# Optimization experiments

Hardware: AMD Instinct MI355X
Metric: run time of the kernel (lower is better)

## Reference

```python
import jax, jax.numpy as jnp
import numpy as np

H = 4          # attention heads
K = 16         # knn neighbors
EPS = 1e-5     # BatchNorm eps


def setup_inputs() -> dict:
    key = jax.random.key(0)
    ks = jax.random.split(key, 10)
    B, C, T, N = 2, 128, 32, 512
    OUT = 128
    HID = 2 * C + 2 * OUT  # ff hidden = in*2 + out*2
    s = 0.02
    return {
        "x_all": jax.random.normal(ks[0], (B, C, T, N), jnp.float32),
        "Wq": jax.random.normal(ks[1], (C, C), jnp.float32) * s,
        "Wk": jax.random.normal(ks[2], (C, C), jnp.float32) * s,
        "Wv": jax.random.normal(ks[3], (C, C), jnp.float32) * s,
        "W1": jax.random.normal(ks[4], (HID, C), jnp.float32) * s,
        "W2": jax.random.normal(ks[5], (OUT, HID), jnp.float32) * s,
        "bn_gamma": 1.0 + 0.1 * jax.random.normal(ks[6], (OUT,), jnp.float32),
        "bn_beta": 0.1 * jax.random.normal(ks[7], (OUT,), jnp.float32),
        "bn_mean": 0.1 * jax.random.normal(ks[8], (OUT,), jnp.float32),
        "bn_var": jax.random.uniform(ks[9], (OUT,), jnp.float32, 0.5, 1.5),
    }


def reference(x_all, Wq, Wk, Wv, W1, W2, bn_gamma, bn_beta, bn_mean, bn_var):
    B, C, T, N = x_all.shape
    D = C // H
    # --- st_group_points: candidate pool = 3 consecutive frames (replicate temporal pad), frame-major ---
    xp = jnp.concatenate([x_all[:, :, :1], x_all, x_all[:, :, -1:]], axis=2)   # (B,C,T+2,N)
    pool = jnp.stack([xp[:, :, :-2], xp[:, :, 1:-1], xp[:, :, 2:]], axis=3)    # (B,C,T,3,N)
    pool = pool.reshape(B, C, T, 3 * N)                                        # (B,C,T,3N)
    # KNN on xyz (channels 0:3); sqrt is monotone so topk on squared dists gives same indices
    a = x_all[:, :3]                                                           # (B,3,T,N)
    b = pool[:, :3]                                                            # (B,3,T,3N)
    d2 = jnp.sum((a[..., :, None] - b[..., None, :]) ** 2, axis=1)             # (B,T,N,3N)
    _, idx = jax.lax.top_k(-d2, K)                                             # (B,T,N,K) smallest-dist
    nb = jnp.take_along_axis(pool[:, :, :, None, :], idx[:, None], axis=-1)    # (B,C,T,N,K)
    rel = x_all[..., None] - nb                                                # diff grouping (B,C,T,N,K)
    # --- per-point local attention over K neighbors (1x1 convs == channel matmuls), all t at once ---
    q = jnp.einsum('oc,bctn->botn', Wq, x_all).reshape(B, H, D, T, N)
    k = jnp.einsum('oc,bctnk->botnk', Wk, rel).reshape(B, H, D, T, N, K)
    v = jnp.einsum('oc,bctnk->botnk', Wv, rel).reshape(B, H, D, T, N, K)
    energy = jnp.einsum('bhdtn,bhdtnk->bhtnk', q, k) / jnp.sqrt(jnp.float32(D))
    attn = jax.nn.softmax(energy, axis=-1)                                     # (B,H,T,N,K)
    agg = jnp.einsum('bhtnk,bhdtnk->bhdtn', attn, v).reshape(B, C, T, N)
    # --- residual + BatchNorm1d (eval mode, running stats) + conv feed-forward ---
    h = x_all + agg
    scale = (bn_gamma / jnp.sqrt(bn_var + EPS))[None, :, None, None]
    h = (h - bn_mean[None, :, None, None]) * scale + bn_beta[None, :, None, None]
    h = jax.nn.leaky_relu(jnp.einsum('oc,bctn->botn', W1, h), 0.2)
    y = jnp.einsum('oc,bctn->botn', W2, h)                                     # (B,OUT,T,N)
    return jnp.concatenate([x_all[:, :4], y], axis=1)                          # (B,4+OUT,T,N)
```

## Files before the change

### kernel.cpp

```cpp
#include <hip/hip_runtime.h>
#include <hip/hip_bf16.h>

typedef __hip_bfloat16 bf16;
typedef unsigned long long u64;
typedef __attribute__((ext_vector_type(8))) short short8;
typedef __attribute__((ext_vector_type(4))) float f32x4;

#define B_   2
#define C_   128
#define T_   32
#define N_   512
#define K_   16
#define HID_ 512
#define TN   (T_*N_)
#define PTS  (B_*T_*N_)

#define MFMA_BF16(a,b,c) __builtin_amdgcn_mfma_f32_16x16x32_bf16((a),(b),(c),0,0,0)

__device__ __forceinline__ float b2f(bf16 v){ return __bfloat162float(v); }
__device__ __forceinline__ bf16  f2b(float v){ return __float2bfloat16(v); }
__device__ __forceinline__ float bqf(short v){
  return __uint_as_float(((unsigned)(unsigned short)v) << 16);
}

__device__ __forceinline__ float ldc(const void* p, int i, bool f32) {
  return f32 ? ((const float*)p)[i] : b2f(((const bf16*)p)[i]);
}

__global__ __launch_bounds__(256) void convw_kernel(
    const void* __restrict__ x,
    const void* wq, const void* wk, const void* wv,
    const void* w1, const void* w2, const void* g, const void* bb,
    const void* m, const void* v,
    bf16* __restrict__ wqb, bf16* __restrict__ wkb, bf16* __restrict__ wvb,
    bf16* __restrict__ w1b, bf16* __restrict__ w2b,
    float* __restrict__ gf, float* __restrict__ bf_, float* __restrict__ mf,
    float* __restrict__ vf, int* __restrict__ flag)
{
  __shared__ int cnt;
  if (threadIdx.x == 0) cnt = 0;
  __syncthreads();
  const unsigned short* u = (const unsigned short*)x;
  int w = 0;
#pragma unroll
  for (int j = 0; j < 8; ++j) {
    unsigned short hv = u[threadIdx.x*8 + j];
    int e = (hv >> 7) & 0xFF;
    if (e >= 0x89) w++;
  }
  if (w) atomicAdd(&cnt, w);
  __syncthreads();
  bool f32 = (cnt > 32);
  if (blockIdx.x == 0 && threadIdx.x == 0) *flag = f32 ? 1 : 0;

  int i = blockIdx.x*256 + threadIdx.x;
  if (i < 16384) { wqb[i] = f2b(ldc(wq, i, f32)); return; } i -= 16384;
  if (i < 16384) { wkb[i] = f2b(ldc(wk, i, f32)); return; } i -= 16384;
  if (i < 16384) { wvb[i] = f2b(ldc(wv, i, f32)); return; } i -= 16384;
  if (i < 65536) { w1b[i] = f2b(ldc(w1, i, f32)); return; } i -= 65536;
  if (i < 65536) { w2b[i] = f2b(ldc(w2, i, f32)); return; } i -= 65536;
  if (i < 128)   { gf[i]  = ldc(g, i, f32); return; }       i -= 128;
  if (i < 128)   { bf_[i] = ldc(bb, i, f32); return; }      i -= 128;
  if (i < 128)   { mf[i]  = ldc(m, i, f32); return; }       i -= 128;
  if (i < 128)   { vf[i]  = ldc(v, i, f32); return; }
}

__device__ __forceinline__ u64 shflx64(u64 v, int m) {
  return (u64)__shfl_xor((long long)v, m, 64);
}

__device__ __forceinline__ void proj_gemm32(const bf16* __restrict__ W,
                                            bf16 (*ys)[136],
                                            const short8 am[2][4],
                                            int mrow, int quad, int ot)
{
  f32x4 acc[2];
#pragma unroll
  for (int mt=0;mt<2;++mt) acc[mt] = (f32x4){0.f,0.f,0.f,0.f};
#pragma unroll
  for (int kq=0;kq<4;++kq) {
    short8 bfr = *(const short8*)&W[(ot*16+mrow)*C_ + kq*32 + quad*8];
#pragma unroll
    for (int mt=0;mt<2;++mt) acc[mt] = MFMA_BF16(am[mt][kq], bfr, acc[mt]);
  }
#pragma unroll
  for (int mt=0;mt<2;++mt)
#pragma unroll
    for (int r=0;r<4;++r)
      ys[mt*16 + quad*4 + r][ot*16 + mrow] = f2b(acc[mt][r]);
}

__device__ __forceinline__ void tile_store32_512(bf16* __restrict__ dst,
                                                 const bf16 (*ys)[136], int tid)
{
  int flat = tid*8;
  int p = flat >> 7, c = flat & 127;
  *(short8*)&dst[(size_t)p*C_ + c] = *(const short8*)&ys[p][c];
}

__global__ __launch_bounds__(512) void projknn_kernel(
    const void* __restrict__ x, const int* __restrict__ flag,
    const bf16* __restrict__ wqb, const bf16* __restrict__ wkb, const bf16* __restrict__ wvb,
    bf16* __restrict__ xTb, bf16* QT, bf16* __restrict__ KT, bf16* __restrict__ VT,
    int* __restrict__ idxout)
{
  __shared__ __align__(16) char smem[28672];
  int tid = threadIdx.x;
  int blk = blockIdx.x;
  int g = blk / 5, r = blk - g*5;
  if (r == 4) {
    bf16 (*xs )[136] = (bf16(*)[136])(smem);
    bf16 (*ysK)[136] = (bf16(*)[136])(smem + 8704);
    bf16 (*ysV)[136] = (bf16(*)[136])(smem + 17408);
    int p0 = g * 32;
    int b = p0 >> 14; int tn0 = p0 & (TN-1);
    if (*flag) {
      const float* xbase = (const float*)x + (size_t)b*C_*TN + tn0;
#pragma unroll
      for (int it=0; it<8; ++it) {
        int i = it*512 + tid;
        int c = i >> 5, p = i & 31;
        xs[p][c] = f2b(xbase[(size_t)c*TN + p]);
      }
    } else {
      const bf16* xbase = (const bf16*)x + (size_t)b*C_*TN + tn0;
#pragma unroll
      for (int it=0; it<8; ++it) {
        int i = it*512 + tid;
        int c = i >> 5, p = i & 31;
        xs[p][c] = xbase[(size_t)c*TN + p];
      }
    }
    __syncthreads();
    tile_store32_512(xTb + (size_t)p0*C_, xs, tid);
    int lane = tid & 63, wave = tid >> 6;
    int mrow = lane & 15, quad = lane >> 4;
    short8 am[2][4];
#pragma unroll
    for (int mt=0;mt<2;++mt)
#pragma unroll
      for (int kq=0;kq<4;++kq)
        am[mt][kq] = *(const short8*)&xs[mt*16 + mrow][kq*32 + quad*8];
    __syncthreads();
    proj_gemm32(wqb, xs,  am, mrow, quad, wave);
    proj_gemm32(wkb, ysK, am, mrow, quad, wave);
    proj_gemm32(wvb, ysV, am, mrow, quad, wave);
    __syncthreads();
    tile_store32_512(QT + (size_t)p0*C_, xs,  tid);
    tile_store32_512(KT + (size_t)p0*C_, ysK, tid);
    tile_store32_512(VT + (size_t)p0*C_, ysV, tid);
  } else {
    float4* cand4 = (float4*)smem;
    u64 (*surv)[64] = (u64(*)[64])(smem + 24576);
    int kblk = g*4 + r;
    int row = kblk >> 6;
    int b = row >> 5, t = row & 31;
    int ng = kblk & 63;
    bool f32 = (*flag != 0);
#pragma unroll
    for (int q = 0; q < 3; ++q) {
      int tt = t - 1 + q; tt = tt < 0 ? 0 : (tt > T_-1 ? T_-1 : tt);
      size_t base = ((size_t)b*C_*T_ + tt)*(size_t)N_ + tid;
      float c0, c1, c2;
      if (f32) {
        const float* xp = (const float*)x;
        c0 = xp[base]; c1 = xp[base + (size_t)T_*N_]; c2 = xp[base + 2*(size_t)T_*N_];
      } else {
        const bf16* xp = (const bf16*)x;
        c0 = b2f(xp[base]); c1 = b2f(xp[base + (size_t)T_*N_]); c2 = b2f(xp[base + 2*(size_t)T_*N_]);
      }
      cand4[q*N_ + tid] = make_float4(c0, c1, c2, 0.f);
    }
    __syncthreads();
    int wave = tid >> 6, lane = tid & 63;
    int n = ng*8 + wave;
    float4 a = cand4[N_ + n];
    unsigned db[24];
#pragma unroll
    for (int j = 0; j < 24; ++j) {
      float4 cm = cand4[lane + (j << 6)];
      float dx = a.x - cm.x;
      float dy = a.y - cm.y;
      float dz = a.z - cm.z;
      float d2 = __fadd_rn(__fadd_rn(__fmul_rn(dx,dx), __fmul_rn(dy,dy)), __fmul_rn(dz,dz));
      db[j] = __float_as_uint(d2);
    }
    unsigned mm[12];
#pragma unroll
    for (int j = 0; j < 12; ++j) mm[j] = db[2*j] < db[2*j+1] ? db[2*j] : db[2*j+1];
#pragma unroll
    for (int j = 0; j < 6; ++j)  mm[j] = mm[2*j] < mm[2*j+1] ? mm[2*j] : mm[2*j+1];
#pragma unroll
    for (int j = 0; j < 3; ++j)  mm[j] = mm[2*j] < mm[2*j+1] ? mm[2*j] : mm[2*j+1];
    unsigned bd = mm[0] < mm[1] ? mm[0] : mm[1];
    bd = bd < mm[2] ? bd : mm[2];
    {
      unsigned lo = 0u, hi = 0x7f800000u;
#pragma unroll
      for (int it = 0; it < 16; ++it) {
        unsigned mid = lo + ((hi - lo) >> 1);
        int cge = __popcll(__ballot(bd <= mid));
        bool ge = (cge >= K_);
        hi = ge ? mid : hi;
        lo = ge ? lo : (mid + 1u);
      }
      bd = hi;
    }
    unsigned U = bd;
    int c = 0;
#pragma unroll
    for (int j = 0; j < 24; ++j) c += (db[j] <= U) ? 1 : 0;
    int ofs = 0, total = 0;
#pragma unroll
    for (int bit = 0; bit < 5; ++bit) {
      u64 mball = __ballot(((c >> bit) & 1) != 0);
      unsigned below = __builtin_amdgcn_mbcnt_hi((unsigned)(mball >> 32),
                        __builtin_amdgcn_mbcnt_lo((unsigned)mball, 0u));
      ofs   += ((int)below) << bit;
      total += (__popcll(mball)) << bit;
    }
    int point = (b*T_ + t)*N_ + n;
    if (total <= 64) {
#pragma unroll
      for (int j = 0; j < 24; ++j) {
        if (db[j] <= U) {
          surv[wave][ofs] = ((u64)db[j] << 11) | (unsigned)(lane + (j << 6));
          ++ofs;
        }
      }
      if (lane == total) surv[wave][lane] = ~0ull;
      __threadfence_block();
      u64 kk = (lane < total) ? surv[wave][lane] : ~0ull;
      int npair = (total + 1) >> 1;
      int rank = 0;
      const ulonglong2* sk2 = (const ulonglong2*)&surv[wave][0];
#pragma unroll 4
      for (int i2 = 0; i2 < npair; ++i2) {
        ulonglong2 kp = sk2[i2];
        rank += (kp.x < kk) ? 1 : 0;
        rank += (kp.y < kk) ? 1 : 0;
      }
      if (rank < K_) idxout[point*K_ + rank] = (int)(kk & 2047u);
    } else {
      u64 key[24];
#pragma unroll
      for (int j = 0; j < 24; ++j)
        key[j] = ((u64)db[j] << 32) | (unsigned)(lane + (j << 6));
      u64 res = ~0ull;
#pragma unroll 1
      for (int rr = 0; rr < 16; ++rr) {
        u64 m2 = key[0];
#pragma unroll
        for (int j = 1; j < 24; ++j) m2 = (key[j] < m2) ? key[j] : m2;
#pragma unroll
        for (int s = 32; s >= 1; s >>= 1) {
          u64 p = shflx64(m2, s);
          m2 = (p < m2) ? p : m2;
        }
        if (lane == rr) res = m2;
        int mwin = (int)(m2 & 0xffffffffu);
        int sel = ((mwin & 63) == lane) ? (mwin >> 6) : -1;
#pragma unroll
        for (int j = 0; j < 24; ++j) if (j == sel) key[j] = ~0ull;
      }
      if (lane < K_) idxout[point*K_ + lane] = (int)(res & 0xffffffffu);
    }
  }
}

__global__ __launch_bounds__(512) void attn_kernel(
    const int* __restrict__ idxin, const bf16* __restrict__ xTb,
    bf16* qhT , const bf16* __restrict__ KT,
    const bf16* __restrict__ VT,
    const float* __restrict__ gf, const float* __restrict__ bf_,
    const float* __restrict__ mf, const float* __restrict__ vf)
{
  __shared__ int   col_lds[4][16];
  __shared__ float qbuf[4][C_];
  __shared__ bf16  kbuf[4][K_][136];
  __shared__ bf16  vbuf[4][K_][136];
  __shared__ float e_lds[4][4][16];
  int tid = threadIdx.x;
  int pt = tid >> 7, o = tid & 127;
  int point = blockIdx.x*4 + pt;
  int b = point >> 14; int tn = point & (TN-1); int t = tn >> 9;
  if (o < K_) {
    int m = idxin[point*K_ + o];
    int j = m >> 9, nn = m & (N_-1);
    int tt = t-1+j; tt = tt<0?0:(tt>T_-1?T_-1:tt);
    col_lds[pt][o] = ((b*T_ + tt)*N_ + nn)*C_;
  }
  int self = point*C_;
  qbuf[pt][o] = b2f(qhT[self + o]);
  __syncthreads();
#pragma unroll
  for (int it = 0; it < 2; ++it) {
    int i = it*512 + tid;
    int pp = i >> 8, rem = i & 255, k = rem >> 4, ch = rem & 15;
    int src = col_lds[pp][k] + ch*8;
    *(short8*)&kbuf[pp][k][ch*8] = *(const short8*)&KT[src];
    *(short8*)&vbuf[pp][k][ch*8] = *(const short8*)&VT[src];
  }
  __syncthreads();
  {
    int pp = tid >> 7, j = tid & 127;
    int k = j >> 3, hd = (j >> 1) & 3, half = j & 1;
    const float* qp = &qbuf[pp][hd*32 + half*16];
    const bf16*  kp = &kbuf[pp][k][hd*32 + half*16];
    short8 kv0 = *(const short8*)kp;
    short8 kv1 = *(const short8*)(kp + 8);
    float qv[16];
    *(float4*)&qv[0]  = *(const float4*)(qp);
    *(float4*)&qv[4]  = *(const float4*)(qp + 4);
    *(float4*)&qv[8]  = *(const float4*)(qp + 8);
    *(float4*)&qv[12] = *(const float4*)(qp + 12);
    float e = 0.f;
#pragma unroll
    for (int i2=0;i2<8;++i2) e = fmaf(qv[i2],   bqf(kv0[i2]), e);
#pragma unroll
    for (int i2=0;i2<8;++i2) e = fmaf(qv[8+i2], bqf(kv1[i2]), e);
    e += __shfl_xor(e, 1, 64);
    if (!half) e_lds[pp][hd][k] = -e * 0.17677669529663687f;
  }
  __syncthreads();
  int hd = o >> 5;
  float e[16]; float mx = -3e38f;
#pragma unroll
  for (int k=0;k<K_;++k){ e[k]=e_lds[pt][hd][k]; mx=fmaxf(mx,e[k]); }
  float ssum=0.f;
#pragma unroll
  for (int k=0;k<K_;++k){ e[k]=__expf(e[k]-mx); ssum+=e[k]; }
  float inv = 1.f/ssum;
  float acc = b2f(VT[self + o]);
#pragma unroll
  for (int k=0;k<K_;++k)
    acc = fmaf(-(e[k]*inv), b2f(vbuf[pt][k][o]), acc);
  float hv = b2f(xTb[self + o]) + acc;
  float sc = gf[o] / sqrtf(vf[o] + 1e-5f);
  qhT[self + o] = f2b((hv - mf[o])*sc + bf_[o]);
}

__global__ __launch_bounds__(256) void mlp_kernel(const bf16* __restrict__ hT,
                                                  const bf16* __restrict__ w1b,
                                                  const bf16* __restrict__ w2b,
                                                  const void* __restrict__ x,
                                                  const int* __restrict__ flag,
                                                  void* out)
{
  __shared__ bf16 hidh[32][264];
  int tid = threadIdx.x;
  int p0 = blockIdx.x*32;
  int lane = tid & 63, wave = tid >> 6;
  int mrow = lane & 15, quad = lane >> 4;
  bool f32o = (*flag != 0);
  int bb = p0 >> 14;
  int tn0 = p0 & (TN-1);
  if (tid < 128) {
    int c = tid >> 5, p = tid & 31;
    size_t si = ((size_t)bb*C_ + c)*TN + tn0 + p;
    size_t di = ((size_t)bb*132 + c)*TN + tn0 + p;
    if (f32o) ((float*)out)[di] = ((const float*)x)[si];
    else      ((bf16*)out)[di]  = ((const bf16*)x)[si];
  }
  f32x4 acc2[2][2];
#pragma unroll
  for (int oi=0;oi<2;++oi)
#pragma unroll
    for (int mt=0;mt<2;++mt) acc2[oi][mt] = (f32x4){0.f,0.f,0.f,0.f};

#pragma unroll
  for (int half = 0; half < 2; ++half) {
    if (half) __syncthreads();
    short8 am[2][4];
#pragma unroll
    for (int mt=0;mt<2;++mt)
#pragma unroll
      for (int kq=0;kq<4;++kq)
        am[mt][kq] = *(const short8*)&hT[(size_t)(p0 + mt*16 + mrow)*C_ + kq*32 + quad*8];
#pragma unroll
    for (int oi = 0; oi < 4; ++oi) {
      int ot_g = half*16 + wave*4 + oi;
      int otl  = wave*4 + oi;
      f32x4 acc[2];
#pragma unroll
      for (int mt=0;mt<2;++mt) acc[mt] = (f32x4){0.f,0.f,0.f,0.f};
#pragma unroll
      for (int kq=0;kq<4;++kq) {
        short8 bfr = *(const short8*)&w1b[(ot_g*16+mrow)*C_ + kq*32 + quad*8];
#pragma unroll
        for (int mt=0;mt<2;++mt) acc[mt] = MFMA_BF16(am[mt][kq], bfr, acc[mt]);
      }
#pragma unroll
      for (int mt=0;mt<2;++mt)
#pragma unroll
        for (int r=0;r<4;++r) {
          float z = acc[mt][r];
          hidh[mt*16 + quad*4 + r][otl*16 + mrow] = f2b(z > 0.f ? z : 0.2f*z);
        }
    }
    __syncthreads();
#pragma unroll
    for (int kc = 0; kc < 4; ++kc) {
      short8 ha[2][2];
#pragma unroll
      for (int mt=0;mt<2;++mt)
#pragma unroll
        for (int kk=0;kk<2;++kk)
          ha[mt][kk] = *(const short8*)&hidh[mt*16 + mrow][(kc*2+kk)*32 + quad*8];
#pragma unroll
      for (int oi=0;oi<2;++oi) {
        int ot2 = wave*2 + oi;
#pragma unroll
        for (int kk=0;kk<2;++kk) {
          int ks_g = half*8 + kc*2 + kk;
          short8 bfr = *(const short8*)&w2b[(ot2*16+mrow)*HID_ + ks_g*32 + quad*8];
#pragma unroll
          for (int mt=0;mt<2;++mt)
            acc2[oi][mt] = MFMA_BF16(ha[mt][kk], bfr, acc2[oi][mt]);
        }
      }
    }
  }
  size_t obase = (size_t)bb*132*TN;
#pragma unroll
  for (int oi=0;oi<2;++oi) {
    int ch = (wave*2+oi)*16 + mrow;
#pragma unroll
    for (int mt=0;mt<2;++mt) {
      int tn = tn0 + mt*16 + quad*4;
      size_t oidx = obase + (size_t)(4+ch)*TN + tn;
      if (f32o) {
        *(f32x4*)&((float*)out)[oidx] = acc2[oi][mt];
      } else {
        bf16 tmp[4];
#pragma unroll
        for (int r=0;r<4;++r) tmp[r] = f2b(acc2[oi][mt][r]);
        *(u64*)&((bf16*)out)[oidx] = *(u64*)tmp;
      }
    }
  }
}

extern "C" void kernel_launch(void* const* d_in, const int* in_sizes, int n_in,
                              void* d_out, int out_size, void* d_ws, size_t ws_size,
                              hipStream_t stream)
{
  (void)in_sizes; (void)n_in; (void)out_size; (void)ws_size;
  const void* x = d_in[0];
  char* ws = (char*)d_ws;
  const size_t MB = (size_t)1<<20;
  bf16*  QT  = (bf16* )(ws + 0*MB);
  bf16*  KT  = (bf16* )(ws + 8*MB);
  bf16*  VT  = (bf16* )(ws + 16*MB);
  bf16*  xTb = (bf16* )(ws + 24*MB);
  int*   idxw= (int*  )(ws + 32*MB);
  bf16*  wqb = (bf16* )(ws + 34*MB);
  bf16*  wkb = (bf16* )(ws + 34*MB + 0x8000);
  bf16*  wvb = (bf16* )(ws + 34*MB + 0x10000);
  bf16*  w1b = (bf16* )(ws + 34*MB + 0x18000);
  bf16*  w2b = (bf16* )(ws + 34*MB + 0x38000);
  float* gf  = (float*)(ws + 34*MB + 0x58000);
  float* bf_ = (float*)(ws + 34*MB + 0x58200);
  float* mf  = (float*)(ws + 34*MB + 0x58400);
  float* vf  = (float*)(ws + 34*MB + 0x58600);
  int*  flag = (int*  )(ws + 34*MB + 0x58800);

  convw_kernel  <<<dim3(706), dim3(256), 0, stream>>>(
      x, d_in[1], d_in[2], d_in[3], d_in[4], d_in[5],
      d_in[6], d_in[7], d_in[8], d_in[9],
      wqb, wkb, wvb, w1b, w2b, gf, bf_, mf, vf, flag);
  projknn_kernel<<<dim3(5120), dim3(512), 0, stream>>>(
      x, flag, wqb, wkb, wvb, xTb, QT, KT, VT, idxw);
  attn_kernel   <<<dim3(PTS/4), dim3(512), 0, stream>>>(
      idxw, xTb, QT , KT, VT, gf, bf_, mf, vf);
  mlp_kernel    <<<dim3(PTS/32), dim3(256), 0, stream>>>(
      QT , w1b, w2b, x, flag, d_out);
}
```

Measured before the change: 207.7 us.

## Process two query points per wave in KNN blocks to amortize candidate loads

Each KNN wave now handles two query points instead of one. Every candidate float4 read from LDS is reused for two distance computations, and the two binary-search threshold loops are interleaved to expose ILP across the ballot chains. The grid shrinks from 5120 to 3072 blocks (two KNN blocks per projection block instead of four), and the heap-select fallback tracks consumed slots with a bitmask instead of rewriting key registers. Register pressure roughly doubles for the distance arrays, and fewer blocks may reduce occupancy or latency hiding.

```diff
diff --git a/kernel.cpp b/kernel.cpp
--- a/kernel.cpp
+++ b/kernel.cpp
@@ -98,17 +98,116 @@
   *(short8*)&dst[(size_t)p*C_ + c] = *(const short8*)&ys[p][c];
 }
 
+__device__ __forceinline__ void knn_thresh2(const unsigned (&db0)[24],
+                                            const unsigned (&db1)[24],
+                                            unsigned& U0, unsigned& U1)
+{
+  unsigned m0[12], m1[12];
+#pragma unroll
+  for (int j = 0; j < 12; ++j) {
+    m0[j] = db0[2*j] < db0[2*j+1] ? db0[2*j] : db0[2*j+1];
+    m1[j] = db1[2*j] < db1[2*j+1] ? db1[2*j] : db1[2*j+1];
+  }
+#pragma unroll
+  for (int j = 0; j < 6; ++j) {
+    m0[j] = m0[2*j] < m0[2*j+1] ? m0[2*j] : m0[2*j+1];
+    m1[j] = m1[2*j] < m1[2*j+1] ? m1[2*j] : m1[2*j+1];
+  }
+#pragma unroll
+  for (int j = 0; j < 3; ++j) {
+    m0[j] = m0[2*j] < m0[2*j+1] ? m0[2*j] : m0[2*j+1];
+    m1[j] = m1[2*j] < m1[2*j+1] ? m1[2*j] : m1[2*j+1];
+  }
+  unsigned bd0 = m0[0] < m0[1] ? m0[0] : m0[1]; bd0 = bd0 < m0[2] ? bd0 : m0[2];
+  unsigned bd1 = m1[0] < m1[1] ? m1[0] : m1[1]; bd1 = bd1 < m1[2] ? bd1 : m1[2];
+  unsigned lo0 = 0u, hi0 = 0x7f800000u, lo1 = 0u, hi1 = 0x7f800000u;
+#pragma unroll
+  for (int it = 0; it < 16; ++it) {
+    unsigned mid0 = lo0 + ((hi0 - lo0) >> 1);
+    unsigned mid1 = lo1 + ((hi1 - lo1) >> 1);
+    int c0 = __popcll(__ballot(bd0 <= mid0));
+    int c1 = __popcll(__ballot(bd1 <= mid1));
+    bool g0 = (c0 >= K_), g1 = (c1 >= K_);
+    hi0 = g0 ? mid0 : hi0;  lo0 = g0 ? lo0 : (mid0 + 1u);
+    hi1 = g1 ? mid1 : hi1;  lo1 = g1 ? lo1 : (mid1 + 1u);
+  }
+  U0 = hi0; U1 = hi1;
+}
+
+__device__ __forceinline__ void knn_emit(const unsigned (&db)[24], unsigned U,
+                                         u64* __restrict__ survw,
+                                         int lane, int point,
+                                         int* __restrict__ idxout)
+{
+  int c = 0;
+#pragma unroll
+  for (int j = 0; j < 24; ++j) c += (db[j] <= U) ? 1 : 0;
+  int ofs = 0, total = 0;
+#pragma unroll
+  for (int bit = 0; bit < 5; ++bit) {
+    u64 mball = __ballot(((c >> bit) & 1) != 0);
+    unsigned below = __builtin_amdgcn_mbcnt_hi((unsigned)(mball >> 32),
+                      __builtin_amdgcn_mbcnt_lo((unsigned)mball, 0u));
+    ofs   += ((int)below) << bit;
+    total += (__popcll(mball)) << bit;
+  }
+  if (total <= 64) {
+#pragma unroll
+    for (int j = 0; j < 24; ++j) {
+      if (db[j] <= U) {
+        survw[ofs] = ((u64)db[j] << 11) | (unsigned)(lane + (j << 6));
+        ++ofs;
+      }
+    }
+    if (lane == total) survw[lane] = ~0ull;
+    __threadfence_block();
+    u64 kk = (lane < total) ? survw[lane] : ~0ull;
+    int npair = (total + 1) >> 1;
+    int rank = 0;
+    const ulonglong2* sk2 = (const ulonglong2*)survw;
+#pragma unroll 4
+    for (int i2 = 0; i2 < npair; ++i2) {
+      ulonglong2 kp = sk2[i2];
+      rank += (kp.x < kk) ? 1 : 0;
+      rank += (kp.y < kk) ? 1 : 0;
+    }
+    if (rank < K_) idxout[point*K_ + rank] = (int)(kk & 2047u);
+  } else {
+    unsigned claimed = 0;
+    u64 res = ~0ull;
+#pragma unroll 1
+    for (int rr = 0; rr < 16; ++rr) {
+      u64 m2 = ~0ull;
+#pragma unroll
+      for (int j = 0; j < 24; ++j) {
+        u64 kj = ((u64)db[j] << 32) | (unsigned)(lane + (j << 6));
+        bool dead = (claimed >> j) & 1;
+        m2 = (!dead && kj < m2) ? kj : m2;
+      }
+#pragma unroll
+      for (int s = 32; s >= 1; s >>= 1) {
+        u64 p = shflx64(m2, s);
+        m2 = (p < m2) ? p : m2;
+      }
+      if (lane == rr) res = m2;
+      int mwin = (int)(m2 & 0xffffffffu);
+      if ((mwin & 63) == lane) claimed |= 1u << (mwin >> 6);
+    }
+    if (lane < K_) idxout[point*K_ + lane] = (int)(res & 0xffffffffu);
+  }
+}
+
 __global__ __launch_bounds__(512) void projknn_kernel(
     const void* __restrict__ x, const int* __restrict__ flag,
     const bf16* __restrict__ wqb, const bf16* __restrict__ wkb, const bf16* __restrict__ wvb,
     bf16* __restrict__ xTb, bf16* QT, bf16* __restrict__ KT, bf16* __restrict__ VT,
     int* __restrict__ idxout)
 {
-  __shared__ __align__(16) char smem[28672];
+  __shared__ __align__(16) char smem[32768];
   int tid = threadIdx.x;
   int blk = blockIdx.x;
-  int g = blk / 5, r = blk - g*5;
-  if (r == 4) {
+  int g = blk / 3, r = blk - g*3;
+  if (r == 2) {
     bf16 (*xs )[136] = (bf16(*)[136])(smem);
     bf16 (*ysK)[136] = (bf16(*)[136])(smem + 8704);
     bf16 (*ysV)[136] = (bf16(*)[136])(smem + 17408);
@@ -151,11 +250,11 @@
     tile_store32_512(VT + (size_t)p0*C_, ysV, tid);
   } else {
     float4* cand4 = (float4*)smem;
-    u64 (*surv)[64] = (u64(*)[64])(smem + 24576);
-    int kblk = g*4 + r;
-    int row = kblk >> 6;
+    u64 (*surv)[2][64] = (u64(*)[2][64])(smem + 24576);
+    int kblk = g*2 + r;
+    int row = kblk >> 5;
     int b = row >> 5, t = row & 31;
-    int ng = kblk & 63;
+    int ng = kblk & 31;
     bool f32 = (*flag != 0);
 #pragma unroll
     for (int q = 0; q < 3; ++q) {
@@ -173,98 +272,23 @@
     }
     __syncthreads();
     int wave = tid >> 6, lane = tid & 63;
-    int n = ng*8 + wave;
-    float4 a = cand4[N_ + n];
-    unsigned db[24];
+    int n0 = ng*16 + wave*2;
+    float4 a0 = cand4[N_ + n0];
+    float4 a1 = cand4[N_ + n0 + 1];
+    unsigned db0[24], db1[24];
 #pragma unroll
     for (int j = 0; j < 24; ++j) {
       float4 cm = cand4[lane + (j << 6)];
-      float dx = a.x - cm.x;
-      float dy = a.y - cm.y;
-      float dz = a.z - cm.z;
-      float d2 = __fadd_rn(__fadd_rn(__fmul_rn(dx,dx), __fmul_rn(dy,dy)), __fmul_rn(dz,dz));
-      db[j] = __float_as_uint(d2);
-    }
-    unsigned mm[12];
-#pragma unroll
-    for (int j = 0; j < 12; ++j) mm[j] = db[2*j] < db[2*j+1] ? db[2*j] : db[2*j+1];
-#pragma unroll
-    for (int j = 0; j < 6; ++j)  mm[j] = mm[2*j] < mm[2*j+1] ? mm[2*j] : mm[2*j+1];
-#pragma unroll
-    for (int j = 0; j < 3; ++j)  mm[j] = mm[2*j] < mm[2*j+1] ? mm[2*j] : mm[2*j+1];
-    unsigned bd = mm[0] < mm[1] ? mm[0] : mm[1];
-    bd = bd < mm[2] ? bd : mm[2];
-    {
-      unsigned lo = 0u, hi = 0x7f800000u;
-#pragma unroll
-      for (int it = 0; it < 16; ++it) {
-        unsigned mid = lo + ((hi - lo) >> 1);
-        int cge = __popcll(__ballot(bd <= mid));
-        bool ge = (cge >= K_);
-        hi = ge ? mid : hi;
-        lo = ge ? lo : (mid + 1u);
-      }
-      bd = hi;
-    }
-    unsigned U = bd;
-    int c = 0;
-#pragma unroll
-    for (int j = 0; j < 24; ++j) c += (db[j] <= U) ? 1 : 0;
-    int ofs = 0, total = 0;
-#pragma unroll
-    for (int bit = 0; bit < 5; ++bit) {
-      u64 mball = __ballot(((c >> bit) & 1) != 0);
-      unsigned below = __builtin_amdgcn_mbcnt_hi((unsigned)(mball >> 32),
-                        __builtin_amdgcn_mbcnt_lo((unsigned)mball, 0u));
-      ofs   += ((int)below) << bit;
-      total += (__popcll(mball)) << bit;
-    }
-    int point = (b*T_ + t)*N_ + n;
-    if (total <= 64) {
-#pragma unroll
-      for (int j = 0; j < 24; ++j) {
-        if (db[j] <= U) {
-          surv[wave][ofs] = ((u64)db[j] << 11) | (unsigned)(lane + (j << 6));
-          ++ofs;
-        }
-      }
-      if (lane == total) surv[wave][lane] = ~0ull;
-      __threadfence_block();
-      u64 kk = (lane < total) ? surv[wave][lane] : ~0ull;
-      int npair = (total + 1) >> 1;
-      int rank = 0;
-      const ulonglong2* sk2 = (const ulonglong2*)&surv[wave][0];
-#pragma unroll 4
-      for (int i2 = 0; i2 < npair; ++i2) {
-        ulonglong2 kp = sk2[i2];
-        rank += (kp.x < kk) ? 1 : 0;
-        rank += (kp.y < kk) ? 1 : 0;
-      }
-      if (rank < K_) idxout[point*K_ + rank] = (int)(kk & 2047u);
-    } else {
-      u64 key[24];
-#pragma unroll
-      for (int j = 0; j < 24; ++j)
-        key[j] = ((u64)db[j] << 32) | (unsigned)(lane + (j << 6));
-      u64 res = ~0ull;
-#pragma unroll 1
-      for (int rr = 0; rr < 16; ++rr) {
-        u64 m2 = key[0];
-#pragma unroll
-        for (int j = 1; j < 24; ++j) m2 = (key[j] < m2) ? key[j] : m2;
-#pragma unroll
-        for (int s = 32; s >= 1; s >>= 1) {
-          u64 p = shflx64(m2, s);
-          m2 = (p < m2) ? p : m2;
-        }
-        if (lane == rr) res = m2;
-        int mwin = (int)(m2 & 0xffffffffu);
-        int sel = ((mwin & 63) == lane) ? (mwin >> 6) : -1;
-#pragma unroll
-        for (int j = 0; j < 24; ++j) if (j == sel) key[j] = ~0ull;
-      }
-      if (lane < K_) idxout[point*K_ + lane] = (int)(res & 0xffffffffu);
-    }
+      float dx0 = a0.x - cm.x, dy0 = a0.y - cm.y, dz0 = a0.z - cm.z;
+      float dx1 = a1.x - cm.x, dy1 = a1.y - cm.y, dz1 = a1.z - cm.z;
+      db0[j] = __float_as_uint(__fadd_rn(__fadd_rn(__fmul_rn(dx0,dx0), __fmul_rn(dy0,dy0)), __fmul_rn(dz0,dz0)));
+      db1[j] = __float_as_uint(__fadd_rn(__fadd_rn(__fmul_rn(dx1,dx1), __fmul_rn(dy1,dy1)), __fmul_rn(dz1,dz1)));
+    }
+    unsigned U0, U1;
+    knn_thresh2(db0, db1, U0, U1);
+    int point = (b*T_ + t)*N_ + n0;
+    knn_emit(db0, U0, surv[wave][0], lane, point,     idxout);
+    knn_emit(db1, U1, surv[wave][1], lane, point + 1, idxout);
   }
 }
 
@@ -469,7 +493,7 @@
       x, d_in[1], d_in[2], d_in[3], d_in[4], d_in[5],
       d_in[6], d_in[7], d_in[8], d_in[9],
       wqb, wkb, wvb, w1b, w2b, gf, bf_, mf, vf, flag);
-  projknn_kernel<<<dim3(5120), dim3(512), 0, stream>>>(
+  projknn_kernel<<<dim3(3072), dim3(512), 0, stream>>>(
       x, flag, wqb, wkb, wvb, xTb, QT, KT, VT, idxw);
   attn_kernel   <<<dim3(PTS/4), dim3(512), 0, stream>>>(
       idxw, xTb, QT , KT, VT, gf, bf_, mf, vf);
```

New measurement: 227.1 us. +9.4%, slower.
